# Performance work log

Hardware: AMD Instinct MI355X
Metric: run time of the kernel (lower is better)

Reference implementation:

```python
import jax, jax.numpy as jnp
import numpy as np

B, S, D, F, H, E = 2, 1024, 1024, 4096, 16, 8
EPS = 1e-5


def _layernorm(x, w, b):
    m = jnp.mean(x, -1, keepdims=True)
    v = jnp.var(x, -1, keepdims=True)
    return (x - m) * jax.lax.rsqrt(v + EPS) * w + b


def _rope(x):
    # rotary embedding applied over full embed dim (split-half convention)
    b, s, d = x.shape
    half = d // 2
    inv = 1.0 / (10000.0 ** (jnp.arange(half, dtype=jnp.float32) / half))
    ang = jnp.arange(s, dtype=jnp.float32)[:, None] * inv[None, :]  # [S, half]
    cos, sin = jnp.cos(ang), jnp.sin(ang)
    x1, x2 = x[..., :half], x[..., half:]
    return jnp.concatenate([x1 * cos - x2 * sin, x1 * sin + x2 * cos], -1)


def setup_inputs() -> dict:
    key = jax.random.key(0)
    ks = jax.random.split(key, 9)
    sc = 0.02
    return {
        "x": jax.random.normal(ks[0], (B, S, D), jnp.float32),
        "ln1_w": jnp.ones((D,), jnp.float32),
        "ln1_b": jnp.zeros((D,), jnp.float32),
        "ln2_w": jnp.ones((D,), jnp.float32),
        "ln2_b": jnp.zeros((D,), jnp.float32),
        "w_qkv": jax.random.normal(ks[1], (3 * D, D), jnp.float32) * sc,
        "b_qkv": jnp.zeros((3 * D,), jnp.float32),
        "w_out": jax.random.normal(ks[2], (D, D), jnp.float32) * sc,
        "b_out": jnp.zeros((D,), jnp.float32),
        "w_router": jax.random.normal(ks[3], (D, E), jnp.float32) * sc,
        "wi": jax.random.normal(ks[4], (E, D, F), jnp.float32) * sc,  # per-expert wi (no bias)
        "wo": jax.random.normal(ks[5], (E, F // 2, D), jnp.float32) * sc,  # swiglu halves ffn dim
    }


def reference(x, ln1_w, ln1_b, ln2_w, ln2_b, w_qkv, b_qkv, w_out, b_out, w_router, wi, wo):
    # ---- pre-norm self-attention block ----
    residual = x
    h = _layernorm(x, ln1_w, ln1_b)
    h = _rope(h)
    qkv = h @ w_qkv.T + b_qkv  # [B,S,3D]
    q, k, v = jnp.split(qkv, 3, axis=-1)
    hd = D // H
    to_heads = lambda t: t.reshape(B, S, H, hd).transpose(0, 2, 1, 3)
    q, k, v = to_heads(q), to_heads(k), to_heads(v)
    scale = 1.0 / np.sqrt(hd).astype(np.float32)
    att = jax.nn.softmax(jnp.einsum('bhqd,bhkd->bhqk', q, k) * scale, axis=-1)
    o = jnp.einsum('bhqk,bhkd->bhqd', att, v).transpose(0, 2, 1, 3).reshape(B, S, D)
    o = o @ w_out.T + b_out
    x = residual + o  # attn dropout is identity at eval

    # ---- pre-norm sparse MoE FFN block ----
    residual = x
    h = _layernorm(x, ln2_w, ln2_b)
    # top-1 router in float32
    logits = h.astype(jnp.float32) @ w_router  # [B,S,E]
    probs = jax.nn.softmax(logits, axis=-1)
    mask = jax.nn.one_hot(jnp.argmax(probs, -1), E, dtype=h.dtype)  # expert_mask
    gate = probs.astype(h.dtype) * mask  # router_probs * expert_mask, [B,S,E]
    # dense all-expert compute, masked combine (same math as gather/scatter loop)
    hid = jnp.einsum('bsd,edf->bsef', h, wi)  # [B,S,E,F]
    a, g = jnp.split(hid, 2, axis=-1)
    act = jax.nn.silu(a) * g  # SwiGLU, [B,S,E,F/2]
    y = jnp.einsum('bsef,efd,bse->bsd', act, wo, gate)
    x = residual + y
    return x, logits
```

## Files before the change

kernel.cpp:

```cpp
#include <hip/hip_runtime.h>
#include <hip/hip_bf16.h>
#include <math.h>

#define BB 2
#define SS 1024
#define DD 1024
#define FF 4096
#define HH 16
#define EE 8
#define MM (BB*SS)
#define MAX_TILES 24
#define MAX_TILES2 40

typedef __attribute__((ext_vector_type(8))) short bf16x8;
typedef __attribute__((ext_vector_type(8))) short s16x8;
typedef __attribute__((ext_vector_type(4))) float f32x4;

#define OFF_WIT  ((size_t)0)
#define OFF_WOT  ((size_t)67108864)
#define OFF_WQH  ((size_t)100663296)
#define OFF_WQL  ((size_t)106954752)
#define OFF_WOH  ((size_t)113246208)
#define OFF_WOL  ((size_t)115343360)
#define OFF_H1H  ((size_t)117440512)
#define OFF_H1L  ((size_t)121634816)
#define OFF_QKV  ((size_t)125829120)
#define OFF_OH   ((size_t)150994944)
#define OFF_OL   ((size_t)155189248)
#define OFF_X2   ((size_t)159383552)
#define OFF_H2B  ((size_t)167772160)
#define OFF_ACT  ((size_t)171966464)
#define OFF_GATE ((size_t)180879360)
#define OFF_EID  ((size_t)180887552)
#define OFF_PERM ((size_t)180895744)
#define OFF_CNT  ((size_t)180903936)
#define OFF_FILL ((size_t)180903968)
#define OFF_NT   ((size_t)180904000)
#define OFF_TE   ((size_t)180904192)
#define OFF_TS   ((size_t)180904320)
#define OFF_TR   ((size_t)180904448)
#define OFF_TE2  ((size_t)180904576)
#define OFF_TS2  ((size_t)180904768)
#define OFF_TR2  ((size_t)180904960)
#define OFF_NT2  ((size_t)180905152)
#define OFF_KSH  OFF_WQH
#define OFF_KSL  (OFF_WQH + 4194304)
#define OFF_VTH  OFF_H1H
#define OFF_VTL  OFF_H1L

__device__ __forceinline__ void gload16(const void* g, void* l) {
    __builtin_amdgcn_global_load_lds(
        (const __attribute__((address_space(1))) unsigned int*)g,
        (__attribute__((address_space(3))) unsigned int*)l, 16, 0, 0);
}

__device__ __forceinline__ short bfh(float v) {
    __hip_bfloat16 h = __float2bfloat16(v);
    return *(short*)&h;
}
__device__ __forceinline__ float bf2f(short s) {
    __hip_bfloat16 h = *(__hip_bfloat16*)&s;
    return __bfloat162float(h);
}

__device__ __forceinline__ void split_write(float v, __hip_bfloat16* hp, __hip_bfloat16* lp, size_t idx) {
    __hip_bfloat16 h = __float2bfloat16(v);
    hp[idx] = h;
    lp[idx] = __float2bfloat16(v - __bfloat162float(h));
}

__device__ __forceinline__ void tcvt64_body(const float* __restrict__ in, __hip_bfloat16* __restrict__ out,
                                            int R, int C, int r0, int c0, float* tile ) {
    int t = threadIdx.x;
    {
        int ri = t >> 2, cj = (t & 3) * 16;
        const float* ip = &in[(size_t)(r0 + ri) * C + c0 + cj];
#pragma unroll
        for (int k = 0; k < 4; ++k) {
            float4 v = *(const float4*)(ip + k * 4);
            tile[ri * 65 + cj + k * 4 + 0] = v.x;
            tile[ri * 65 + cj + k * 4 + 1] = v.y;
            tile[ri * 65 + cj + k * 4 + 2] = v.z;
            tile[ri * 65 + cj + k * 4 + 3] = v.w;
        }
    }
    __syncthreads();
    {
        int co = t >> 2, rj = (t & 3) * 16;
        bf16x8 v8a, v8b;
#pragma unroll
        for (int q = 0; q < 8; ++q) v8a[q] = bfh(tile[(rj + q) * 65 + co]);
#pragma unroll
        for (int q = 0; q < 8; ++q) v8b[q] = bfh(tile[(rj + 8 + q) * 65 + co]);
        __hip_bfloat16* op = &out[(size_t)(c0 + co) * R + r0 + rj];
        *(bf16x8*)op = v8a;
        *(bf16x8*)(op + 8) = v8b;
    }
}

__global__ void k_phase0(const float* __restrict__ x, const float* __restrict__ ln1w,
                         const float* __restrict__ ln1b,
                         __hip_bfloat16* __restrict__ h1H, __hip_bfloat16* __restrict__ h1L,
                         const float* __restrict__ w_qkv, __hip_bfloat16* __restrict__ wqH,
                         __hip_bfloat16* __restrict__ wqL) {
    __shared__ __align__(16) float smem[1032];
    int bid = blockIdx.x, t = threadIdx.x;
    if (bid < 2048) {
        int m = bid, s = m & (SS - 1);
        float* row = smem;
        float* red = smem + 1024;
        const float* xp = x + (size_t)m * DD;
        float sum = 0.f, sumsq = 0.f;
#pragma unroll
        for (int l = 0; l < 4; ++l) {
            int i = t + l * 256;
            float v = xp[i];
            row[i] = v;
            sum += v; sumsq += v * v;
        }
#pragma unroll
        for (int off = 32; off; off >>= 1) {
            sum   += __shfl_xor(sum, off);
            sumsq += __shfl_xor(sumsq, off);
        }
        int wid = t >> 6, lane = t & 63;
        if (lane == 0) { red[wid] = sum; red[4 + wid] = sumsq; }
        __syncthreads();
        sum   = red[0] + red[1] + red[2] + red[3];
        sumsq = red[4] + red[5] + red[6] + red[7];
        float mean = sum * (1.f / DD);
        float var  = sumsq * (1.f / DD) - mean * mean;
        float rstd = rsqrtf(var + 1e-5f);
        size_t base = (size_t)m * DD;
        const float kln = logf(10000.f) / 512.f;
#pragma unroll
        for (int l = 0; l < 2; ++l) {
            int i = t + l * 256;
            float n1 = (row[i]       - mean) * rstd * ln1w[i]       + ln1b[i];
            float n2 = (row[i + 512] - mean) * rstd * ln1w[i + 512] + ln1b[i + 512];
            float inv = expf(-(float)i * kln);
            float ang = (float)s * inv;
            float c = cosf(ang), sn = sinf(ang);
            split_write(n1 * c - n2 * sn,  h1H, h1L, base + i);
            split_write(n1 * sn + n2 * c, h1H, h1L, base + i + 512);
        }
    } else {
        int idx = (bid - 2048) * 256 + t;
        float4 v = ((const float4*)w_qkv)[idx];
        split_write(v.x, wqH, wqL, (size_t)idx * 4 + 0);
        split_write(v.y, wqH, wqL, (size_t)idx * 4 + 1);
        split_write(v.z, wqH, wqL, (size_t)idx * 4 + 2);
        split_write(v.w, wqH, wqL, (size_t)idx * 4 + 3);
    }
}

__global__ void k_qkv_mega(const __hip_bfloat16* __restrict__ Ah, const __hip_bfloat16* __restrict__ Al,
                           const __hip_bfloat16* __restrict__ Bh, const __hip_bfloat16* __restrict__ Bl,
                           const float* __restrict__ bias, float* __restrict__ Cf,
                           const float* __restrict__ wi, __hip_bfloat16* __restrict__ wiT,
                           const float* __restrict__ w_out, __hip_bfloat16* __restrict__ woH,
                           __hip_bfloat16* __restrict__ woL) {
    __shared__ __align__(16) char smem[32768];
    int bid = blockIdx.x;
    const int t = threadIdx.x;
    if (bid < 384) {
        const int N = 3072, K = DD;
        short* AsH = (short*)smem;
        short* AsL = (short*)(smem + 8192);
        short* BsH = (short*)(smem + 16384);
        short* BsL = (short*)(smem + 24576);
        int n0 = (bid % 24) * 128, m0 = (bid / 24) * 128;
        const int w = t >> 6, lane = t & 63;
        const int wr = w >> 1, wc = w & 1;
        const int sid = w * 64 + lane;

        f32x4 acc[4][4] = {};

        for (int k0 = 0; k0 < K; k0 += 32) {
#pragma unroll
            for (int j = 0; j < 2; ++j) {
                int id = j * 256 + sid;
                int rrow = id >> 2, sl = id & 3;
                int slog = sl ^ ((rrow >> 1) & 3);
                size_t lbase = (size_t)(j * 256 + w * 64) * 8;
                size_t gaoff = (size_t)(m0 + rrow) * K + k0 + slog * 8;
                gload16(Ah + gaoff, &AsH[lbase]);
                gload16(Al + gaoff, &AsL[lbase]);
                size_t gboff = (size_t)(n0 + rrow) * K + k0 + slog * 8;
                gload16(Bh + gboff, &BsH[lbase]);
                gload16(Bl + gboff, &BsL[lbase]);
            }
            __syncthreads();
            bf16x8 ah[4], al[4], bh[4], bl[4];
#pragma unroll
            for (int i = 0; i < 4; ++i) {
                int ra = wr * 64 + i * 16 + (lane & 15);
                int pa = (lane >> 4) ^ ((ra >> 1) & 3);
                ah[i] = *(const bf16x8*)&AsH[ra * 32 + pa * 8];
                al[i] = *(const bf16x8*)&AsL[ra * 32 + pa * 8];
                int rb = wc * 64 + i * 16 + (lane & 15);
                int pb = (lane >> 4) ^ ((rb >> 1) & 3);
                bh[i] = *(const bf16x8*)&BsH[rb * 32 + pb * 8];
                bl[i] = *(const bf16x8*)&BsL[rb * 32 + pb * 8];
            }
#pragma unroll
            for (int i = 0; i < 4; ++i)
#pragma unroll
                for (int n = 0; n < 4; ++n) {
                    acc[i][n] = __builtin_amdgcn_mfma_f32_16x16x32_bf16(ah[i], bh[n], acc[i][n], 0, 0, 0);
                    acc[i][n] = __builtin_amdgcn_mfma_f32_16x16x32_bf16(ah[i], bl[n], acc[i][n], 0, 0, 0);
                    acc[i][n] = __builtin_amdgcn_mfma_f32_16x16x32_bf16(al[i], bh[n], acc[i][n], 0, 0, 0);
                }
            __syncthreads();
        }

        int cn = n0 + wc * 64 + (lane & 15);
#pragma unroll
        for (int i = 0; i < 4; ++i) {
#pragma unroll
            for (int n = 0; n < 4; ++n) {
                int col = cn + n * 16;
#pragma unroll
                for (int q = 0; q < 4; ++q) {
                    int r = wr * 64 + i * 16 + (lane >> 4) * 4 + q;
                    Cf[(size_t)(m0 + r) * N + col] = acc[i][n][q] + bias[col];
                }
            }
        }
    } else if (bid < 8576) {
        int j = bid - 384;
        int e = j >> 10, rem = j & 1023;
        int ry = rem >> 6, cx = rem & 63;
        tcvt64_body(wi + (size_t)e * DD * FF, wiT + (size_t)e * DD * FF,
                    1024, 4096, ry * 64, cx * 64, (float*)smem);
    } else {
        int idx = (bid - 8576) * 256 + t;
        float4 v = ((const float4*)w_out)[idx];
        split_write(v.x, woH, woL, (size_t)idx * 4 + 0);
        split_write(v.y, woH, woL, (size_t)idx * 4 + 1);
        split_write(v.z, woH, woL, (size_t)idx * 4 + 2);
        split_write(v.w, woH, woL, (size_t)idx * 4 + 3);
    }
}

__global__ void k_oproj64(const __hip_bfloat16* __restrict__ Ah, const __hip_bfloat16* __restrict__ Al,
                          const __hip_bfloat16* __restrict__ Bh, const __hip_bfloat16* __restrict__ Bl,
                          const float* __restrict__ bias, const float* __restrict__ addsrc,
                          float* __restrict__ Cf, int* __restrict__ zero17) {
    __shared__ __align__(16) short AsH[64 * 32];
    __shared__ __align__(16) short AsL[64 * 32];
    __shared__ __align__(16) short BsH[128 * 32];
    __shared__ __align__(16) short BsL[128 * 32];
    const int N = DD, K = DD;
    int bid = blockIdx.x;
    int m0 = (bid >> 3) * 64, n0 = (bid & 7) * 128;
    const int t = threadIdx.x;
    if (bid == 0 && t < 17) zero17[t] = 0;
    const int w = t >> 6, lane = t & 63;
    const int sid = w * 64 + lane;
    const int g = lane >> 4, r16 = lane & 15;

    f32x4 acc[4][2] = {};

    for (int k0 = 0; k0 < K; k0 += 32) {
        {
            int rrow = sid >> 2, sl = sid & 3;
            int slog = sl ^ ((rrow >> 1) & 3);
            size_t lbase = (size_t)(w * 64) * 8;
            size_t gaoff = (size_t)(m0 + rrow) * K + k0 + slog * 8;
            gload16(Ah + gaoff, &AsH[lbase]);
            gload16(Al + gaoff, &AsL[lbase]);
        }
#pragma unroll
        for (int j = 0; j < 2; ++j) {
            int id = j * 256 + sid;
            int rrow = id >> 2, sl = id & 3;
            int slog = sl ^ ((rrow >> 1) & 3);
            size_t lbase = (size_t)(j * 256 + w * 64) * 8;
            size_t gboff = (size_t)(n0 + rrow) * K + k0 + slog * 8;
            gload16(Bh + gboff, &BsH[lbase]);
            gload16(Bl + gboff, &BsL[lbase]);
        }
        __syncthreads();
        bf16x8 ah[4], al[4], bh[2], bl[2];
#pragma unroll
        for (int i = 0; i < 4; ++i) {
            int ra = i * 16 + r16;
            int pa = g ^ ((ra >> 1) & 3);
            ah[i] = *(const bf16x8*)&AsH[ra * 32 + pa * 8];
            al[i] = *(const bf16x8*)&AsL[ra * 32 + pa * 8];
        }
#pragma unroll
        for (int n = 0; n < 2; ++n) {
            int rb = w * 32 + n * 16 + r16;
            int pb = g ^ ((rb >> 1) & 3);
            bh[n] = *(const bf16x8*)&BsH[rb * 32 + pb * 8];
            bl[n] = *(const bf16x8*)&BsL[rb * 32 + pb * 8];
        }
#pragma unroll
        for (int i = 0; i < 4; ++i)
#pragma unroll
            for (int n = 0; n < 2; ++n) {
                acc[i][n] = __builtin_amdgcn_mfma_f32_16x16x32_bf16(ah[i], bh[n], acc[i][n], 0, 0, 0);
                acc[i][n] = __builtin_amdgcn_mfma_f32_16x16x32_bf16(ah[i], bl[n], acc[i][n], 0, 0, 0);
                acc[i][n] = __builtin_amdgcn_mfma_f32_16x16x32_bf16(al[i], bh[n], acc[i][n], 0, 0, 0);
            }
        __syncthreads();
    }

#pragma unroll
    for (int i = 0; i < 4; ++i) {
#pragma unroll
        for (int n = 0; n < 2; ++n) {
            int col = n0 + w * 32 + n * 16 + r16;
#pragma unroll
            for (int q = 0; q < 4; ++q) {
                int r = m0 + i * 16 + g * 4 + q;
                Cf[(size_t)r * N + col] =
                    acc[i][n][q] + bias[col] + addsrc[(size_t)r * N + col];
            }
        }
    }
}

__global__ void k_moe_up(const __hip_bfloat16* __restrict__ A,
                         const __hip_bfloat16* __restrict__ Bt,
                         __hip_bfloat16* __restrict__ act,
                         const int* __restrict__ perm,
                         const int* __restrict__ te, const int* __restrict__ ts,
                         const int* __restrict__ tr, const int* __restrict__ ntl,
                         const float* __restrict__ wo, __hip_bfloat16* __restrict__ woT) {
    __shared__ __align__(16) char smem[17408];
    int bid = blockIdx.x;
    const int t = threadIdx.x;
    if (bid >= 768) {
        int j = bid - 768;
        int e = j >> 9, rem = j & 511;
        int ry = rem >> 4, cx = rem & 15;
        tcvt64_body(wo + (size_t)e * 2048 * 1024, woT + (size_t)e * 2048 * 1024,
                    2048, 1024, ry * 64, cx * 64, (float*)smem);
        return;
    }
    short* As = (short*)smem;
    short* Bs = (short*)(smem + 8192);
    int* permS = (int*)(smem + 16384);
    int tile = bid / 32;
    if (tile >= *ntl) return;
    int e = te[tile], rs = ts[tile], rows = tr[tile];
    if (t < 128) permS[t] = (t < rows) ? perm[rs + t] : 0;
    __syncthreads();
    int c0 = (bid & 31) * 64;
    const int w = t >> 6, lane = t & 63;
    const int wr = w >> 1, wc = w & 1;
    const int sid = w * 64 + lane;
    const int g = lane >> 4, r16 = lane & 15;

    const __hip_bfloat16* Bp = Bt + (size_t)e * FF * DD;

    f32x4 acc[4][4] = {};

    for (int k0 = 0; k0 < DD; k0 += 32) {
#pragma unroll
        for (int j = 0; j < 2; ++j) {
            int id = j * 256 + sid;
            int rrow = id >> 2, sl = id & 3;
            int slog = sl ^ ((rrow >> 1) & 3);
            size_t lbase = (size_t)(j * 256 + w * 64) * 8;
            gload16(A + (size_t)permS[rrow] * DD + k0 + slog * 8, &As[lbase]);
            int q = rrow >> 4, rr = rrow & 15;
            int wrow = c0 + (q >> 2) * 32 + ((q & 3) >> 1) * 16 + rr + (q & 1) * 2048;
            gload16(Bp + (size_t)wrow * DD + k0 + slog * 8, &Bs[lbase]);
        }
        __syncthreads();
        bf16x8 af[4], bfr[4];
#pragma unroll
        for (int i = 0; i < 4; ++i) {
            int ra = wr * 64 + i * 16 + r16;
            int pa = g ^ ((ra >> 1) & 3);
            af[i] = *(const bf16x8*)&As[ra * 32 + pa * 8];
            int rb = wc * 64 + i * 16 + r16;
            int pb = g ^ ((rb >> 1) & 3);
            bfr[i] = *(const bf16x8*)&Bs[rb * 32 + pb * 8];
        }
#pragma unroll
        for (int i = 0; i < 4; ++i)
#pragma unroll
            for (int n = 0; n < 4; ++n)
                acc[i][n] = __builtin_amdgcn_mfma_f32_16x16x32_bf16(af[i], bfr[n], acc[i][n], 0, 0, 0);
        __syncthreads();
    }

#pragma unroll
    for (int i = 0; i < 4; ++i) {
#pragma unroll
        for (int p2 = 0; p2 < 2; ++p2) {
            int col = c0 + wc * 32 + p2 * 16 + r16;
#pragma unroll
            for (int q = 0; q < 4; ++q) {
                int r = wr * 64 + i * 16 + g * 4 + q;
                if (r < rows) {
                    float a  = acc[i][2 * p2][q];
                    float gv = acc[i][2 * p2 + 1][q];
                    act[(size_t)(rs + r) * 2048 + col] =
                        __float2bfloat16((a / (1.f + expf(-a))) * gv);
                }
            }
        }
    }
}

__global__ void k_moe_dn(const __hip_bfloat16* __restrict__ A,
                         const __hip_bfloat16* __restrict__ Bt,
                         const float* __restrict__ addsrc, float* __restrict__ Cf,
                         const int* __restrict__ perm,
                         const int* __restrict__ te2, const int* __restrict__ ts2,
                         const int* __restrict__ tr2, const int* __restrict__ ntl2,
                         const float* __restrict__ gate) {
    __shared__ __align__(16) short As[64 * 32];
    __shared__ __align__(16) short Bs[128 * 32];
    __shared__ int permS[64];
    int tile = blockIdx.y;
    if (tile >= *ntl2) return;
    int e = te2[tile], rs = ts2[tile], rows = tr2[tile];
    const int t = threadIdx.x;
    if (t < 64) permS[t] = (t < rows) ? perm[rs + t] : 0;
    __syncthreads();
    int n0 = blockIdx.x * 128;
    const int w = t >> 6, lane = t & 63;
    const int sid = w * 64 + lane;
    const int g = lane >> 4, r16 = lane & 15;
    const int K = FF / 2;

    const __hip_bfloat16* Bp = Bt + (size_t)e * DD * (FF / 2);

    f32x4 acc[4][2] = {};

    for (int k0 = 0; k0 < K; k0 += 32) {
        {
            int rrow = sid >> 2, sl = sid & 3;
            int slog = sl ^ ((rrow >> 1) & 3);
            size_t lbase = (size_t)(w * 64) * 8;
            gload16(A + (size_t)(rs + rrow) * K + k0 + slog * 8, &As[lbase]);
        }
#pragma unroll
        for (int j = 0; j < 2; ++j) {
            int id = j * 256 + sid;
            int rrow = id >> 2, sl = id & 3;
            int slog = sl ^ ((rrow >> 1) & 3);
            size_t lbase = (size_t)(j * 256 + w * 64) * 8;
            gload16(Bp + (size_t)(n0 + rrow) * K + k0 + slog * 8, &Bs[lbase]);
        }
        __syncthreads();
        bf16x8 af[4], bfr[2];
#pragma unroll
        for (int i = 0; i < 4; ++i) {
            int ra = i * 16 + r16;
            int pa = g ^ ((ra >> 1) & 3);
            af[i] = *(const bf16x8*)&As[ra * 32 + pa * 8];
        }
#pragma unroll
        for (int n = 0; n < 2; ++n) {
            int rb = w * 32 + n * 16 + r16;
            int pb = g ^ ((rb >> 1) & 3);
            bfr[n] = *(const bf16x8*)&Bs[rb * 32 + pb * 8];
        }
#pragma unroll
        for (int i = 0; i < 4; ++i)
#pragma unroll
            for (int n = 0; n < 2; ++n)
                acc[i][n] = __builtin_amdgcn_mfma_f32_16x16x32_bf16(af[i], bfr[n], acc[i][n], 0, 0, 0);
        __syncthreads();
    }

#pragma unroll
    for (int i = 0; i < 4; ++i) {
#pragma unroll
        for (int n = 0; n < 2; ++n) {
            int col = n0 + w * 32 + n * 16 + r16;
#pragma unroll
            for (int q = 0; q < 4; ++q) {
                int r = i * 16 + g * 4 + q;
                if (r >= rows) continue;
                int tok = permS[r];
                Cf[(size_t)tok * DD + col] = addsrc[(size_t)tok * DD + col] + gate[tok] * acc[i][n][q];
            }
        }
    }
}

__global__ void k_prep(const float* __restrict__ qkv, short* __restrict__ KH, short* __restrict__ KL,
                       short* __restrict__ VH, short* __restrict__ VL) {
    __shared__ float tile[64][65];
    int b = blockIdx.z, h = blockIdx.y, s0 = blockIdx.x * 64;
    int t = threadIdx.x;
    int row = t >> 2, c0 = (t & 3) * 16;
    const float* kp = qkv + (size_t)(b * SS + s0 + row) * 3072 + 1024 + h * 64 + c0;
    const float* vp = kp + 1024;
    {
        size_t krow = ((size_t)(b * HH + h) * SS + s0 + row) * 64;
        int key = (s0 + row) & 7;
#pragma unroll
        for (int g2 = 0; g2 < 2; ++g2) {
            s16x8 hv, lv;
#pragma unroll
            for (int j = 0; j < 8; ++j) {
                float v = kp[g2 * 8 + j];
                short hh = bfh(v);
                hv[j] = hh; lv[j] = bfh(v - bf2f(hh));
            }
            int p = ((c0 >> 3) + g2) ^ key;
            *(s16x8*)&KH[krow + p * 8] = hv;
            *(s16x8*)&KL[krow + p * 8] = lv;
        }
    }
#pragma unroll
    for (int j = 0; j < 16; ++j) tile[row][c0 + j] = vp[j];
    __syncthreads();
    {
        int d = t >> 2, sc = (t & 3) * 16;
        size_t vrow = ((size_t)(b * HH + h) * 64 + d) * SS + s0;
        int key = d & 7;
#pragma unroll
        for (int g2 = 0; g2 < 2; ++g2) {
            s16x8 hv, lv;
#pragma unroll
            for (int j = 0; j < 8; ++j) {
                float v = tile[sc + g2 * 8 + j][d];
                short hh = bfh(v);
                hv[j] = hh; lv[j] = bfh(v - bf2f(hh));
            }
            int p = ((sc >> 3) + g2) ^ key;
            *(s16x8*)&VH[vrow + p * 8] = hv;
            *(s16x8*)&VL[vrow + p * 8] = lv;
        }
    }
}

#define LDP 72
__global__ __launch_bounds__(512, 1)
void k_attn_mfma(const float* __restrict__ qkv,
                 const short* __restrict__ KH, const short* __restrict__ KL,
                 const short* __restrict__ VH, const short* __restrict__ VL,
                 __hip_bfloat16* __restrict__ ohi, __hip_bfloat16* __restrict__ olo) {
    __shared__ __align__(16) short Ks[2][64 * 64], Kl2[2][64 * 64], Vs[2][64 * 64], Vl2[2][64 * 64];
    __shared__ __align__(16) short PhS[8][16 * LDP], PlS[8][16 * LDP];
    int id = blockIdx.x;
    int xcd = id & 7, slot = id >> 3;
    int bh = xcd * 4 + (slot >> 3);
    int q0 = (slot & 7) * 128;
    int b = bh >> 4, h = bh & 15;
    int t = threadIdx.x;
    int w = t >> 6, lane = t & 63;
    int g = lane >> 4, r16 = lane & 15;
    int srow = t >> 3, sslot = t & 7;

    const size_t kbase = ((size_t)bh * SS) * 64;
    const size_t vbase = ((size_t)bh * 64) * SS;

    bf16x8 qfh[2], qfl[2];
    {
        const float* qp = qkv + (size_t)(b * SS + q0 + w * 16 + r16) * 3072 + h * 64;
#pragma unroll
        for (int ks = 0; ks < 2; ++ks) {
            float vv[8];
            *(float4*)&vv[0] = *(const float4*)(qp + ks * 32 + g * 8);
            *(float4*)&vv[4] = *(const float4*)(qp + ks * 32 + g * 8 + 4);
#pragma unroll
            for (int j = 0; j < 8; ++j) {
                float sv = vv[j] * 0.125f;
                short hh = bfh(sv);
                qfh[ks][j] = hh;
                qfl[ks][j] = bfh(sv - bf2f(hh));
            }
        }
    }

    float mrun[4], lrun[4];
    f32x4 oacc[4] = {};
#pragma unroll
    for (int q = 0; q < 4; ++q) { mrun[q] = -1e30f; lrun[q] = 0.f; }

    gload16(KH + kbase + (size_t)srow * 64 + sslot * 8, &Ks[0][w * 512]);
    gload16(KL + kbase + (size_t)srow * 64 + sslot * 8, &Kl2[0][w * 512]);
    gload16(VH + vbase + (size_t)srow * SS + sslot * 8, &Vs[0][w * 512]);
    gload16(VL + vbase + (size_t)srow * SS + sslot * 8, &Vl2[0][w * 512]);
    __syncthreads();

    int cur = 0;
    for (int k0 = 0; k0 < SS; k0 += 64) {
        if (k0 + 64 < SS) {
            int kn = k0 + 64;
            gload16(KH + kbase + (size_t)(kn + srow) * 64 + sslot * 8, &Ks[cur ^ 1][w * 512]);
            gload16(KL + kbase + (size_t)(kn + srow) * 64 + sslot * 8, &Kl2[cur ^ 1][w * 512]);
            gload16(VH + vbase + (size_t)srow * SS + kn + sslot * 8,   &Vs[cur ^ 1][w * 512]);
            gload16(VL + vbase + (size_t)srow * SS + kn + sslot * 8,   &Vl2[cur ^ 1][w * 512]);
        }

        f32x4 accs[4] = {};
#pragma unroll
        for (int ks = 0; ks < 2; ++ks) {
            bf16x8 kfh[4], kfl[4];
#pragma unroll
            for (int n = 0; n < 4; ++n) {
                int rb = n * 16 + r16;
                int p = (ks * 4 + g) ^ (r16 & 7);
                kfh[n] = *(const bf16x8*)&Ks[cur][rb * 64 + p * 8];
                kfl[n] = *(const bf16x8*)&Kl2[cur][rb * 64 + p * 8];
            }
            __builtin_amdgcn_s_setprio(1);
#pragma unroll
            for (int n = 0; n < 4; ++n) {
                accs[n] = __builtin_amdgcn_mfma_f32_16x16x32_bf16(qfh[ks], kfh[n], accs[n], 0, 0, 0);
                accs[n] = __builtin_amdgcn_mfma_f32_16x16x32_bf16(qfh[ks], kfl[n], accs[n], 0, 0, 0);
                accs[n] = __builtin_amdgcn_mfma_f32_16x16x32_bf16(qfl[ks], kfh[n], accs[n], 0, 0, 0);
            }
            __builtin_amdgcn_s_setprio(0);
        }

        float mn[4], corr[4], psum[4];
#pragma unroll
        for (int q = 0; q < 4; ++q) {
            float m = fmaxf(fmaxf(accs[0][q], accs[1][q]), fmaxf(accs[2][q], accs[3][q]));
            m = fmaxf(m, __shfl_xor(m, 1));
            m = fmaxf(m, __shfl_xor(m, 2));
            m = fmaxf(m, __shfl_xor(m, 4));
            m = fmaxf(m, __shfl_xor(m, 8));
            mn[q] = fmaxf(mrun[q], m);
            corr[q] = expf(mrun[q] - mn[q]);
            mrun[q] = mn[q];
            psum[q] = 0.f;
        }
#pragma unroll
        for (int n = 0; n < 4; ++n)
#pragma unroll
            for (int q = 0; q < 4; ++q) {
                float p = expf(accs[n][q] - mn[q]);
                psum[q] += p;
                short ph = bfh(p);
                PhS[w][(g * 4 + q) * LDP + n * 16 + r16] = ph;
                PlS[w][(g * 4 + q) * LDP + n * 16 + r16] = bfh(p - bf2f(ph));
            }
#pragma unroll
        for (int q = 0; q < 4; ++q) {
            psum[q] += __shfl_xor(psum[q], 1);
            psum[q] += __shfl_xor(psum[q], 2);
            psum[q] += __shfl_xor(psum[q], 4);
            psum[q] += __shfl_xor(psum[q], 8);
            lrun[q] = lrun[q] * corr[q] + psum[q];
#pragma unroll
            for (int n = 0; n < 4; ++n) oacc[n][q] *= corr[q];
        }

#pragma unroll
        for (int ks = 0; ks < 2; ++ks) {
            bf16x8 vfh[4], vfl[4];
#pragma unroll
            for (int n = 0; n < 4; ++n) {
                int rb = n * 16 + r16;
                int p = (ks * 4 + g) ^ (r16 & 7);
                vfh[n] = *(const bf16x8*)&Vs[cur][rb * 64 + p * 8];
                vfl[n] = *(const bf16x8*)&Vl2[cur][rb * 64 + p * 8];
            }
            bf16x8 pfh = *(const bf16x8*)&PhS[w][r16 * LDP + ks * 32 + g * 8];
            bf16x8 pfl = *(const bf16x8*)&PlS[w][r16 * LDP + ks * 32 + g * 8];
            __builtin_amdgcn_s_setprio(1);
#pragma unroll
            for (int n = 0; n < 4; ++n) {
                oacc[n] = __builtin_amdgcn_mfma_f32_16x16x32_bf16(pfh, vfh[n], oacc[n], 0, 0, 0);
                oacc[n] = __builtin_amdgcn_mfma_f32_16x16x32_bf16(pfh, vfl[n], oacc[n], 0, 0, 0);
                oacc[n] = __builtin_amdgcn_mfma_f32_16x16x32_bf16(pfl, vfh[n], oacc[n], 0, 0, 0);
            }
            __builtin_amdgcn_s_setprio(0);
        }
        __syncthreads();
        cur ^= 1;
    }

    float invl[4];
#pragma unroll
    for (int q = 0; q < 4; ++q) invl[q] = 1.f / lrun[q];
#pragma unroll
    for (int n = 0; n < 4; ++n) {
        int col = h * 64 + n * 16 + r16;
#pragma unroll
        for (int q = 0; q < 4; ++q) {
            int rowg = b * SS + q0 + w * 16 + g * 4 + q;
            split_write(oacc[n][q] * invl[q], ohi, olo, (size_t)rowg * DD + col);
        }
    }
}

__global__ void k_ln2_router(const float* __restrict__ x2, const float* __restrict__ w,
                             const float* __restrict__ b, const float* __restrict__ wr,
                             __hip_bfloat16* __restrict__ h2b, float* __restrict__ logits,
                             float* __restrict__ gate, int* __restrict__ eid,
                             int* __restrict__ counts) {
    int m = blockIdx.x, t = threadIdx.x;
    __shared__ float red[8];
    __shared__ float racc[4][8];
    const float* xp = x2 + (size_t)m * DD;
    float v[4];
    float sum = 0.f, sumsq = 0.f;
#pragma unroll
    for (int l = 0; l < 4; ++l) {
        v[l] = xp[t + l * 256];
        sum += v[l]; sumsq += v[l] * v[l];
    }
#pragma unroll
    for (int off = 32; off; off >>= 1) {
        sum   += __shfl_xor(sum, off);
        sumsq += __shfl_xor(sumsq, off);
    }
    int wid = t >> 6, lane = t & 63;
    if (lane == 0) { red[wid] = sum; red[4 + wid] = sumsq; }
    __syncthreads();
    sum   = red[0] + red[1] + red[2] + red[3];
    sumsq = red[4] + red[5] + red[6] + red[7];
    float mean = sum * (1.f / DD);
    float var  = sumsq * (1.f / DD) - mean * mean;
    float rstd = rsqrtf(var + 1e-5f);
    float acc[EE] = {};
#pragma unroll
    for (int l = 0; l < 4; ++l) {
        int i = t + l * 256;
        float hv = (v[l] - mean) * rstd * w[i] + b[i];
        h2b[(size_t)m * DD + i] = __float2bfloat16(hv);
        const float* wp = wr + (size_t)i * EE;
#pragma unroll
        for (int n = 0; n < EE; ++n) acc[n] += hv * wp[n];
    }
#pragma unroll
    for (int off = 32; off; off >>= 1)
#pragma unroll
        for (int n = 0; n < EE; ++n) acc[n] += __shfl_xor(acc[n], off);
    if (lane == 0)
#pragma unroll
        for (int n = 0; n < EE; ++n) racc[wid][n] = acc[n];
    __syncthreads();
    if (t == 0) {
        float lg[EE];
#pragma unroll
        for (int n = 0; n < EE; ++n) lg[n] = racc[0][n] + racc[1][n] + racc[2][n] + racc[3][n];
        float mx = lg[0]; int best = 0;
#pragma unroll
        for (int n = 1; n < EE; ++n) if (lg[n] > mx) { mx = lg[n]; best = n; }
        float den = 0.f;
#pragma unroll
        for (int n = 0; n < EE; ++n) den += expf(lg[n] - mx);
        gate[m] = 1.f / den;
        eid[m] = best;
        atomicAdd(&counts[best], 1);
#pragma unroll
        for (int n = 0; n < EE; ++n) logits[(size_t)m * EE + n] = lg[n];
    }
}

__global__ void k_offscatter(const int* __restrict__ counts,
                             int* __restrict__ te, int* __restrict__ ts, int* __restrict__ tr,
                             int* __restrict__ ntl,
                             int* __restrict__ te2, int* __restrict__ ts2, int* __restrict__ tr2,
                             int* __restrict__ ntl2,
                             const int* __restrict__ eid,
                             int* __restrict__ fill, int* __restrict__ perm) {
    __shared__ int soffs[EE];
    int t = threadIdx.x;
    if (t == 0) {
        int off = 0, nt = 0, nt2 = 0;
        for (int e = 0; e < EE; ++e) {
            soffs[e] = off;
            int c = counts[e];
            for (int t0 = 0; t0 < c; t0 += 128) {
                te[nt] = e; ts[nt] = off + t0; tr[nt] = (c - t0 < 128) ? (c - t0) : 128; ++nt;
            }
            for (int t0 = 0; t0 < c; t0 += 64) {
                te2[nt2] = e; ts2[nt2] = off + t0; tr2[nt2] = (c - t0 < 64) ? (c - t0) : 64; ++nt2;
            }
            off += c;
        }
        *ntl = nt;
        *ntl2 = nt2;
    }
    __syncthreads();
#pragma unroll
    for (int tok = t; tok < MM; tok += 1024) {
        int e = eid[tok];
        int pos = soffs[e] + atomicAdd(&fill[e], 1);
        perm[pos] = tok;
    }
}

extern "C" void kernel_launch(void* const* d_in, const int* in_sizes, int n_in,
                              void* d_out, int out_size, void* d_ws, size_t ws_size,
                              hipStream_t stream) {
    const float* x     = (const float*)d_in[0];
    const float* ln1w  = (const float*)d_in[1];
    const float* ln1b  = (const float*)d_in[2];
    const float* ln2w  = (const float*)d_in[3];
    const float* ln2b  = (const float*)d_in[4];
    const float* w_qkv = (const float*)d_in[5];
    const float* b_qkv = (const float*)d_in[6];
    const float* w_out = (const float*)d_in[7];
    const float* b_out = (const float*)d_in[8];
    const float* w_rtr = (const float*)d_in[9];
    const float* wi    = (const float*)d_in[10];
    const float* wo    = (const float*)d_in[11];
    float* out = (float*)d_out;

    char* wsb = (char*)d_ws;
    __hip_bfloat16* wiT  = (__hip_bfloat16*)(wsb + OFF_WIT);
    __hip_bfloat16* woT  = (__hip_bfloat16*)(wsb + OFF_WOT);
    __hip_bfloat16* wqH  = (__hip_bfloat16*)(wsb + OFF_WQH);
    __hip_bfloat16* wqL  = (__hip_bfloat16*)(wsb + OFF_WQL);
    __hip_bfloat16* woH  = (__hip_bfloat16*)(wsb + OFF_WOH);
    __hip_bfloat16* woL  = (__hip_bfloat16*)(wsb + OFF_WOL);
    __hip_bfloat16* h1H  = (__hip_bfloat16*)(wsb + OFF_H1H);
    __hip_bfloat16* h1L  = (__hip_bfloat16*)(wsb + OFF_H1L);
    float*          qkvF = (float*)(wsb + OFF_QKV);
    __hip_bfloat16* oH   = (__hip_bfloat16*)(wsb + OFF_OH);
    __hip_bfloat16* oL   = (__hip_bfloat16*)(wsb + OFF_OL);
    float*          x2F  = (float*)(wsb + OFF_X2);
    __hip_bfloat16* h2B  = (__hip_bfloat16*)(wsb + OFF_H2B);
    __hip_bfloat16* actB = (__hip_bfloat16*)(wsb + OFF_ACT);
    short* KSH = (short*)(wsb + OFF_KSH);
    short* KSL = (short*)(wsb + OFF_KSL);
    short* VTH = (short*)(wsb + OFF_VTH);
    short* VTL = (short*)(wsb + OFF_VTL);
    float* gate = (float*)(wsb + OFF_GATE);
    int* eid    = (int*)(wsb + OFF_EID);
    int* perm   = (int*)(wsb + OFF_PERM);
    int* counts = (int*)(wsb + OFF_CNT);
    int* fill   = (int*)(wsb + OFF_FILL);
    int* ntl    = (int*)(wsb + OFF_NT);
    int* te     = (int*)(wsb + OFF_TE);
    int* tsx    = (int*)(wsb + OFF_TS);
    int* trx    = (int*)(wsb + OFF_TR);
    int* te2    = (int*)(wsb + OFF_TE2);
    int* ts2    = (int*)(wsb + OFF_TS2);
    int* tr2    = (int*)(wsb + OFF_TR2);
    int* ntl2   = (int*)(wsb + OFF_NT2);

    k_phase0<<<5120, 256, 0, stream>>>(x, ln1w, ln1b, h1H, h1L, w_qkv, wqH, wqL);
    k_qkv_mega<<<9600, 256, 0, stream>>>(h1H, h1L, wqH, wqL, b_qkv, qkvF,
                                         wi, wiT, w_out, woH, woL);
    k_prep<<<dim3(SS / 64, HH, BB), 256, 0, stream>>>(qkvF, KSH, KSL, VTH, VTL);
    k_attn_mfma<<<256, 512, 0, stream>>>(qkvF, KSH, KSL, VTH, VTL, oH, oL);
    k_oproj64<<<256, 256, 0, stream>>>(oH, oL, woH, woL, b_out, x, x2F, counts);
    k_ln2_router<<<MM, 256, 0, stream>>>(x2F, ln2w, ln2b, w_rtr, h2B,
                                         out + (size_t)MM * DD, gate, eid, counts);
    k_offscatter<<<1, 1024, 0, stream>>>(counts, te, tsx, trx, ntl,
                                         te2, ts2, tr2, ntl2, eid, fill, perm);
    k_moe_up<<<768 + 4096, 256, 0, stream>>>(h2B, wiT, actB, perm, te, tsx, trx, ntl,
                                             wo, woT);
    k_moe_dn<<<dim3(DD / 128, MAX_TILES2), 256, 0, stream>>>(
        actB, woT, x2F, out, perm, te2, ts2, tr2, ntl2, gate);
}
```

Baseline: 316.4 us.

## Shrink QKV GEMM tiles, move w_out split to phase0, single-buffer attention

Moves the w_out hi/lo split conversion from the QKV mega-kernel into the phase-0 kernel. The QKV GEMM tile drops from 128x128 to 64x128, doubling the block count to 768, which shrinks LDS to 24KB and gives each wave a 64x32 slice. The attention kernel drops K/V double buffering in favour of a single buffer with a sync per step, and raises launch_bounds occupancy to 4. This aims for better occupancy and load balance, at the cost of exposing load latency in attention and lowering per-block data reuse in the GEMM.

Result: no change. 320.3 us (+1.2%).

```diff
diff --git a/kernel.cpp b/kernel.cpp
--- a/kernel.cpp
+++ b/kernel.cpp
@@ -102,7 +102,9 @@
                          const float* __restrict__ ln1b,
                          __hip_bfloat16* __restrict__ h1H, __hip_bfloat16* __restrict__ h1L,
                          const float* __restrict__ w_qkv, __hip_bfloat16* __restrict__ wqH,
-                         __hip_bfloat16* __restrict__ wqL) {
+                         __hip_bfloat16* __restrict__ wqL,
+                         const float* __restrict__ w_out, __hip_bfloat16* __restrict__ woH,
+                         __hip_bfloat16* __restrict__ woL) {
     __shared__ __align__(16) float smem[1032];
     int bid = blockIdx.x, t = threadIdx.x;
     if (bid < 2048) {
@@ -144,69 +146,82 @@
             split_write(n1 * c - n2 * sn,  h1H, h1L, base + i);
             split_write(n1 * sn + n2 * c, h1H, h1L, base + i + 512);
         }
-    } else {
+    } else if (bid < 5120) {
         int idx = (bid - 2048) * 256 + t;
         float4 v = ((const float4*)w_qkv)[idx];
         split_write(v.x, wqH, wqL, (size_t)idx * 4 + 0);
         split_write(v.y, wqH, wqL, (size_t)idx * 4 + 1);
         split_write(v.z, wqH, wqL, (size_t)idx * 4 + 2);
         split_write(v.w, wqH, wqL, (size_t)idx * 4 + 3);
+    } else {
+        int idx = (bid - 5120) * 256 + t;
+        float4 v = ((const float4*)w_out)[idx];
+        split_write(v.x, woH, woL, (size_t)idx * 4 + 0);
+        split_write(v.y, woH, woL, (size_t)idx * 4 + 1);
+        split_write(v.z, woH, woL, (size_t)idx * 4 + 2);
+        split_write(v.w, woH, woL, (size_t)idx * 4 + 3);
     }
 }
 
 __global__ void k_qkv_mega(const __hip_bfloat16* __restrict__ Ah, const __hip_bfloat16* __restrict__ Al,
                            const __hip_bfloat16* __restrict__ Bh, const __hip_bfloat16* __restrict__ Bl,
                            const float* __restrict__ bias, float* __restrict__ Cf,
-                           const float* __restrict__ wi, __hip_bfloat16* __restrict__ wiT,
-                           const float* __restrict__ w_out, __hip_bfloat16* __restrict__ woH,
-                           __hip_bfloat16* __restrict__ woL) {
-    __shared__ __align__(16) char smem[32768];
+                           const float* __restrict__ wi, __hip_bfloat16* __restrict__ wiT) {
+    __shared__ __align__(16) char smem[24576];
     int bid = blockIdx.x;
     const int t = threadIdx.x;
-    if (bid < 384) {
+    if (bid < 768) {
         const int N = 3072, K = DD;
         short* AsH = (short*)smem;
-        short* AsL = (short*)(smem + 8192);
-        short* BsH = (short*)(smem + 16384);
-        short* BsL = (short*)(smem + 24576);
-        int n0 = (bid % 24) * 128, m0 = (bid / 24) * 128;
+        short* AsL = (short*)(smem + 4096);
+        short* BsH = (short*)(smem + 8192);
+        short* BsL = (short*)(smem + 16384);
+        int m0 = (bid / 24) * 64, n0 = (bid % 24) * 128;
         const int w = t >> 6, lane = t & 63;
-        const int wr = w >> 1, wc = w & 1;
         const int sid = w * 64 + lane;
-
-        f32x4 acc[4][4] = {};
+        const int g = lane >> 4, r16 = lane & 15;
+
+        f32x4 acc[4][2] = {};
 
         for (int k0 = 0; k0 < K; k0 += 32) {
+            {
+                int rrow = sid >> 2, sl = sid & 3;
+                int slog = sl ^ ((rrow >> 1) & 3);
+                size_t lbase = (size_t)(w * 64) * 8;
+                size_t gaoff = (size_t)(m0 + rrow) * K + k0 + slog * 8;
+                gload16(Ah + gaoff, &AsH[lbase]);
+                gload16(Al + gaoff, &AsL[lbase]);
+            }
 #pragma unroll
             for (int j = 0; j < 2; ++j) {
                 int id = j * 256 + sid;
                 int rrow = id >> 2, sl = id & 3;
                 int slog = sl ^ ((rrow >> 1) & 3);
                 size_t lbase = (size_t)(j * 256 + w * 64) * 8;
-                size_t gaoff = (size_t)(m0 + rrow) * K + k0 + slog * 8;
-                gload16(Ah + gaoff, &AsH[lbase]);
-                gload16(Al + gaoff, &AsL[lbase]);
                 size_t gboff = (size_t)(n0 + rrow) * K + k0 + slog * 8;
                 gload16(Bh + gboff, &BsH[lbase]);
                 gload16(Bl + gboff, &BsL[lbase]);
             }
             __syncthreads();
-            bf16x8 ah[4], al[4], bh[4], bl[4];
+            bf16x8 ah[4], al[4], bh[2], bl[2];
 #pragma unroll
             for (int i = 0; i < 4; ++i) {
-                int ra = wr * 64 + i * 16 + (lane & 15);
-                int pa = (lane >> 4) ^ ((ra >> 1) & 3);
+                int ra = i * 16 + r16;
+                int pa = g ^ ((ra >> 1) & 3);
                 ah[i] = *(const bf16x8*)&AsH[ra * 32 + pa * 8];
                 al[i] = *(const bf16x8*)&AsL[ra * 32 + pa * 8];
-                int rb = wc * 64 + i * 16 + (lane & 15);
-                int pb = (lane >> 4) ^ ((rb >> 1) & 3);
-                bh[i] = *(const bf16x8*)&BsH[rb * 32 + pb * 8];
-                bl[i] = *(const bf16x8*)&BsL[rb * 32 + pb * 8];
+            }
+#pragma unroll
+            for (int n = 0; n < 2; ++n) {
+                int rb = w * 32 + n * 16 + r16;
+                int pb = g ^ ((rb >> 1) & 3);
+                bh[n] = *(const bf16x8*)&BsH[rb * 32 + pb * 8];
+                bl[n] = *(const bf16x8*)&BsL[rb * 32 + pb * 8];
             }
 #pragma unroll
             for (int i = 0; i < 4; ++i)
 #pragma unroll
-                for (int n = 0; n < 4; ++n) {
+                for (int n = 0; n < 2; ++n) {
                     acc[i][n] = __builtin_amdgcn_mfma_f32_16x16x32_bf16(ah[i], bh[n], acc[i][n], 0, 0, 0);
                     acc[i][n] = __builtin_amdgcn_mfma_f32_16x16x32_bf16(ah[i], bl[n], acc[i][n], 0, 0, 0);
                     acc[i][n] = __builtin_amdgcn_mfma_f32_16x16x32_bf16(al[i], bh[n], acc[i][n], 0, 0, 0);
@@ -214,32 +229,24 @@
             __syncthreads();
         }
 
-        int cn = n0 + wc * 64 + (lane & 15);
 #pragma unroll
         for (int i = 0; i < 4; ++i) {
 #pragma unroll
-            for (int n = 0; n < 4; ++n) {
-                int col = cn + n * 16;
+            for (int n = 0; n < 2; ++n) {
+                int col = n0 + w * 32 + n * 16 + r16;
 #pragma unroll
                 for (int q = 0; q < 4; ++q) {
-                    int r = wr * 64 + i * 16 + (lane >> 4) * 4 + q;
-                    Cf[(size_t)(m0 + r) * N + col] = acc[i][n][q] + bias[col];
+                    int r = m0 + i * 16 + g * 4 + q;
+                    Cf[(size_t)r * N + col] = acc[i][n][q] + bias[col];
                 }
             }
         }
-    } else if (bid < 8576) {
-        int j = bid - 384;
+    } else {
+        int j = bid - 768;
         int e = j >> 10, rem = j & 1023;
         int ry = rem >> 6, cx = rem & 63;
         tcvt64_body(wi + (size_t)e * DD * FF, wiT + (size_t)e * DD * FF,
                     1024, 4096, ry * 64, cx * 64, (float*)smem);
-    } else {
-        int idx = (bid - 8576) * 256 + t;
-        float4 v = ((const float4*)w_out)[idx];
-        split_write(v.x, woH, woL, (size_t)idx * 4 + 0);
-        split_write(v.y, woH, woL, (size_t)idx * 4 + 1);
-        split_write(v.z, woH, woL, (size_t)idx * 4 + 2);
-        split_write(v.w, woH, woL, (size_t)idx * 4 + 3);
     }
 }
 
@@ -537,12 +544,12 @@
 }
 
 #define LDP 72
-__global__ __launch_bounds__(512, 1)
+__global__ __launch_bounds__(512, 4)
 void k_attn_mfma(const float* __restrict__ qkv,
                  const short* __restrict__ KH, const short* __restrict__ KL,
                  const short* __restrict__ VH, const short* __restrict__ VL,
                  __hip_bfloat16* __restrict__ ohi, __hip_bfloat16* __restrict__ olo) {
-    __shared__ __align__(16) short Ks[2][64 * 64], Kl2[2][64 * 64], Vs[2][64 * 64], Vl2[2][64 * 64];
+    __shared__ __align__(16) short Ks[64 * 64], Kl2[64 * 64], Vs[64 * 64], Vl2[64 * 64];
     __shared__ __align__(16) short PhS[8][16 * LDP], PlS[8][16 * LDP];
     int id = blockIdx.x;
     int xcd = id & 7, slot = id >> 3;
@@ -580,21 +587,12 @@
 #pragma unroll
     for (int q = 0; q < 4; ++q) { mrun[q] = -1e30f; lrun[q] = 0.f; }
 
-    gload16(KH + kbase + (size_t)srow * 64 + sslot * 8, &Ks[0][w * 512]);
-    gload16(KL + kbase + (size_t)srow * 64 + sslot * 8, &Kl2[0][w * 512]);
-    gload16(VH + vbase + (size_t)srow * SS + sslot * 8, &Vs[0][w * 512]);
-    gload16(VL + vbase + (size_t)srow * SS + sslot * 8, &Vl2[0][w * 512]);
-    __syncthreads();
-
-    int cur = 0;
     for (int k0 = 0; k0 < SS; k0 += 64) {
-        if (k0 + 64 < SS) {
-            int kn = k0 + 64;
-            gload16(KH + kbase + (size_t)(kn + srow) * 64 + sslot * 8, &Ks[cur ^ 1][w * 512]);
-            gload16(KL + kbase + (size_t)(kn + srow) * 64 + sslot * 8, &Kl2[cur ^ 1][w * 512]);
-            gload16(VH + vbase + (size_t)srow * SS + kn + sslot * 8,   &Vs[cur ^ 1][w * 512]);
-            gload16(VL + vbase + (size_t)srow * SS + kn + sslot * 8,   &Vl2[cur ^ 1][w * 512]);
-        }
+        gload16(KH + kbase + (size_t)(k0 + srow) * 64 + sslot * 8, &Ks[w * 512]);
+        gload16(KL + kbase + (size_t)(k0 + srow) * 64 + sslot * 8, &Kl2[w * 512]);
+        gload16(VH + vbase + (size_t)srow * SS + k0 + sslot * 8,   &Vs[w * 512]);
+        gload16(VL + vbase + (size_t)srow * SS + k0 + sslot * 8,   &Vl2[w * 512]);
+        __syncthreads();
 
         f32x4 accs[4] = {};
 #pragma unroll
@@ -604,8 +602,8 @@
             for (int n = 0; n < 4; ++n) {
                 int rb = n * 16 + r16;
                 int p = (ks * 4 + g) ^ (r16 & 7);
-                kfh[n] = *(const bf16x8*)&Ks[cur][rb * 64 + p * 8];
-                kfl[n] = *(const bf16x8*)&Kl2[cur][rb * 64 + p * 8];
+                kfh[n] = *(const bf16x8*)&Ks[rb * 64 + p * 8];
+                kfl[n] = *(const bf16x8*)&Kl2[rb * 64 + p * 8];
             }
             __builtin_amdgcn_s_setprio(1);
 #pragma unroll
@@ -658,8 +656,8 @@
             for (int n = 0; n < 4; ++n) {
                 int rb = n * 16 + r16;
                 int p = (ks * 4 + g) ^ (r16 & 7);
-                vfh[n] = *(const bf16x8*)&Vs[cur][rb * 64 + p * 8];
-                vfl[n] = *(const bf16x8*)&Vl2[cur][rb * 64 + p * 8];
+                vfh[n] = *(const bf16x8*)&Vs[rb * 64 + p * 8];
+                vfl[n] = *(const bf16x8*)&Vl2[rb * 64 + p * 8];
             }
             bf16x8 pfh = *(const bf16x8*)&PhS[w][r16 * LDP + ks * 32 + g * 8];
             bf16x8 pfl = *(const bf16x8*)&PlS[w][r16 * LDP + ks * 32 + g * 8];
@@ -673,7 +671,6 @@
             __builtin_amdgcn_s_setprio(0);
         }
         __syncthreads();
-        cur ^= 1;
     }
 
     float invl[4];
@@ -839,9 +836,9 @@
     int* tr2    = (int*)(wsb + OFF_TR2);
     int* ntl2   = (int*)(wsb + OFF_NT2);
 
-    k_phase0<<<5120, 256, 0, stream>>>(x, ln1w, ln1b, h1H, h1L, w_qkv, wqH, wqL);
-    k_qkv_mega<<<9600, 256, 0, stream>>>(h1H, h1L, wqH, wqL, b_qkv, qkvF,
-                                         wi, wiT, w_out, woH, woL);
+    k_phase0<<<6144, 256, 0, stream>>>(x, ln1w, ln1b, h1H, h1L, w_qkv, wqH, wqL,
+                                       w_out, woH, woL);
+    k_qkv_mega<<<8960, 256, 0, stream>>>(h1H, h1L, wqH, wqL, b_qkv, qkvF, wi, wiT);
     k_prep<<<dim3(SS / 64, HH, BB), 256, 0, stream>>>(qkvF, KSH, KSL, VTH, VTL);
     k_attn_mfma<<<256, 512, 0, stream>>>(qkvF, KSH, KSL, VTH, VTL, oH, oL);
     k_oproj64<<<256, 256, 0, stream>>>(oH, oL, woH, woL, b_out, x, x2F, counts);
```
